# Kernel tuning notes

Measured on AMD Instinct MI355X. Metric: run time of the kernel, lower is better.

The kernel has to match this reference:

```python
import jax, jax.numpy as jnp
import numpy as np

B, N, P, D, K = 32, 512, 25, 128, 64
PROMPT_THRESHOLD = 0.5
T_MTI = 24  # last time patch is masked (module asserts t_mti == [24])


def setup_inputs() -> dict:
    key = jax.random.key(0)
    k1, k2, k3, k4, k5 = jax.random.split(key, 5)
    patches = jax.random.normal(k1, (B, N, P, D), dtype=jnp.float32)
    # kaiming-uniform-like init scale for the embedding tables
    scale = 1.0 / np.sqrt(D)
    u_prompt = jax.random.normal(k2, (K, D), dtype=jnp.float32) * scale
    m_prompt = jax.random.normal(k3, (K, D), dtype=jnp.float32) * scale
    s_mti = jnp.sort(jax.random.randint(k4, (256,), 0, N))
    s_uti = jnp.sort(jax.random.randint(k5, (256,), 0, N))
    return {"patches": patches, "u_prompt": u_prompt, "m_prompt": m_prompt,
            "s_mti": s_mti, "s_uti": s_uti}


def reference(patches, u_prompt, m_prompt, s_mti, s_uti):
    n, p = patches.shape[1], patches.shape[2]
    # multiplicative masks equivalent to score_map[:, s_mti] = 0 and score_map[:, :, 24] = 0
    n_mask = jnp.ones((n,), dtype=patches.dtype).at[s_mti].set(0.0)
    t_mask = jnp.ones((p,), dtype=patches.dtype).at[T_MTI].set(0.0)
    keep = (n_mask[:, None] * t_mask[None, :])[None, :, :, None]  # [1,N,P,1]

    # --- unmasked-prompt pass ---
    su = jax.nn.sigmoid(jnp.einsum('bnpd,kd->bnpk', patches, u_prompt))
    su = su * (su > PROMPT_THRESHOLD).astype(su.dtype) * keep
    out = patches + jnp.einsum('bnpk,kd->bnpd', su, u_prompt)

    # --- masked-prompt pass: score - score_with_keep == score * (1 - keep) ---
    sm = jax.nn.sigmoid(jnp.einsum('bnpd,kd->bnpk', patches, m_prompt))
    sm = sm * (sm > PROMPT_THRESHOLD).astype(sm.dtype) * (1.0 - keep)
    out = out + jnp.einsum('bnpk,kd->bnpd', sm, m_prompt)
    return out
```

## Files before the change

kernel.cpp:

```cpp
#include <hip/hip_runtime.h>


constexpr int NN = 512;
constexpr int PP = 25;
constexpr int DD = 128;
constexpr int KK = 64;
constexpr int THREADS = 512;
constexpr int ROWS = 32 * NN * PP;
constexpr int RPB = THREADS / 4;
constexpr int BLOCKS = ROWS / RPB;

__global__ __launch_bounds__(THREADS, 2)
void ape_kernel(const float* __restrict__ patches,
                const float* __restrict__ u_prompt,
                const float* __restrict__ m_prompt,
                const int* __restrict__ s_mti,
                float* __restrict__ out)
{
    __shared__ float S[2 * KK * DD];
    __shared__ unsigned nmask[NN / 32];

    const int tid = threadIdx.x;
    float4* S4 = reinterpret_cast<float4*>(S);

    if (tid < NN / 32) nmask[tid] = 0u;
    __syncthreads();
    if (tid < 256) {
        int idx = s_mti[tid];
        atomicOr(&nmask[idx >> 5], 1u << (idx & 31));
    }

    {
        const float4* u4 = reinterpret_cast<const float4*>(u_prompt);
        const float4* m4 = reinterpret_cast<const float4*>(m_prompt);
#pragma unroll
        for (int i = 0; i < 4; ++i) {
            int jj = i * THREADS + tid;
            int k = jj >> 5, j = jj & 31;
            int phys = (j & 24) | ((j ^ (j >> 3)) & 7);
            S4[k * 32 + phys]        = u4[jj];
            S4[2048 + k * 32 + phys] = m4[jj];
        }
    }
    __syncthreads();

    const int q = tid & 3;
    const int rl = tid >> 2;
    const int r = blockIdx.x * RPB + rl;
    const int rdp = r / PP;
    const int pp = r - rdp * PP;
    const int n = rdp & (NN - 1);
    const bool masked = (((nmask[n >> 5] >> (n & 31)) & 1u) != 0u) || (pp == 24);
    const int tb = masked ? 2048 : 0;

    int ecol[8];
#pragma unroll
    for (int t = 0; t < 8; ++t) ecol[t] = tb + q * 8 + ((t ^ q) & 7);

    const float4* pr = reinterpret_cast<const float4*>(patches) + (size_t)r * 32 + q * 8;
    float4 row[8], acc[8];
#pragma unroll
    for (int t = 0; t < 8; ++t) {
        row[t] = pr[t];
        acc[t] = row[t];
    }

#pragma unroll 1
    for (int k = 0; k < KK; ++k) {
        const int kb = k * 32;
        float4 e[8];
        float a0 = 0.f, a1 = 0.f, a2 = 0.f, a3 = 0.f;
#pragma unroll
        for (int t = 0; t < 8; ++t) {
            e[t] = S4[kb + ecol[t]];
            a0 = fmaf(row[t].x, e[t].x, a0);
            a1 = fmaf(row[t].y, e[t].y, a1);
            a2 = fmaf(row[t].z, e[t].z, a2);
            a3 = fmaf(row[t].w, e[t].w, a3);
        }
        float lg = (a0 + a1) + (a2 + a3);
        lg += __shfl_xor(lg, 1);
        lg += __shfl_xor(lg, 2);

        float g;
        if (__any(__builtin_fabsf(lg) < 1e-3f)) {
            double dd = 0.0;
#pragma unroll
            for (int t = 0; t < 8; ++t) {
                dd = fma((double)row[t].x, (double)e[t].x, dd);
                dd = fma((double)row[t].y, (double)e[t].y, dd);
                dd = fma((double)row[t].z, (double)e[t].z, dd);
                dd = fma((double)row[t].w, (double)e[t].w, dd);
            }
            dd += __shfl_xor(dd, 1);
            dd += __shfl_xor(dd, 2);
            if (fabs(dd) < 4e-5) {
                g = 0.25f;
            } else if (dd > 0.0) {
                g = __builtin_amdgcn_rcpf(1.0f + __expf(-lg));
            } else {
                g = 0.0f;
            }
        } else {
            g = (lg > 0.0f) ? __builtin_amdgcn_rcpf(1.0f + __expf(-lg)) : 0.0f;
        }

#pragma unroll
        for (int t = 0; t < 8; ++t) {
            acc[t].x = fmaf(g, e[t].x, acc[t].x);
            acc[t].y = fmaf(g, e[t].y, acc[t].y);
            acc[t].z = fmaf(g, e[t].z, acc[t].z);
            acc[t].w = fmaf(g, e[t].w, acc[t].w);
        }
    }

    __syncthreads();
    {
        const int r7 = rl & 7;
        const int wb = rl * 32 + q * 8;
#pragma unroll
        for (int t = 0; t < 8; ++t)
            S4[wb + ((t ^ q ^ r7) & 7)] = acc[t];
    }
    __syncthreads();
    {
        float4* out4 = reinterpret_cast<float4*>(out) + (size_t)blockIdx.x * (RPB * 32);
#pragma unroll
        for (int i = 0; i < 8; ++i) {
            int flat = i * THREADS + tid;
            int rr = flat >> 5, c = flat & 31;
            int qq = c >> 3, tt = c & 7;
            out4[flat] = S4[rr * 32 + qq * 8 + ((tt ^ qq ^ (rr & 7)) & 7)];
        }
    }
}

extern "C" void kernel_launch(void* const* d_in, const int* in_sizes, int n_in,
                              void* d_out, int out_size, void* d_ws, size_t ws_size,
                              hipStream_t stream) {
    const float* patches  = (const float*)d_in[0];
    const float* u_prompt = (const float*)d_in[1];
    const float* m_prompt = (const float*)d_in[2];
    const int*   s_mti    = (const int*)d_in[3];
    float* outp = (float*)d_out;

    ape_kernel<<<BLOCKS, THREADS, 0, stream>>>(patches, u_prompt, m_prompt, s_mti, outp);
}
```

Before: 659.7 us.

## Process two rows per thread sharing the same prompt table to reuse LDS loads

Each thread now handles a pair of rows that share the same mask state (patch j and j+12 of the same (b,n), or the p=24 patches of two adjacent groups). Each LDS prompt vector load is then reused for two dot products and two accumulations, halving LDS traffic per row and halving block count. The shared-memory staged coalesced output write is replaced by direct strided float4 stores from registers. Register pressure roughly doubles for row/acc arrays, which may reduce occupancy or cause spills under the 512-thread launch bound.

```diff
diff --git a/kernel.cpp b/kernel.cpp
--- a/kernel.cpp
+++ b/kernel.cpp
@@ -6,9 +6,10 @@
 constexpr int DD = 128;
 constexpr int KK = 64;
 constexpr int THREADS = 512;
-constexpr int ROWS = 32 * NN * PP;
-constexpr int RPB = THREADS / 4;
-constexpr int BLOCKS = ROWS / RPB;
+constexpr int PAIRS_A = 32 * NN * 12;
+constexpr int PAIRS_B = 32 * NN / 2;
+constexpr int PPB = THREADS / 4;
+constexpr int BLOCKS = (PAIRS_A + PAIRS_B) / PPB;
 
 __global__ __launch_bounds__(THREADS, 2)
 void ape_kernel(const float* __restrict__ patches,
@@ -45,24 +46,35 @@
     __syncthreads();
 
     const int q = tid & 3;
-    const int rl = tid >> 2;
-    const int r = blockIdx.x * RPB + rl;
-    const int rdp = r / PP;
-    const int pp = r - rdp * PP;
-    const int n = rdp & (NN - 1);
-    const bool masked = (((nmask[n >> 5] >> (n & 31)) & 1u) != 0u) || (pp == 24);
+    const int P = blockIdx.x * PPB + (tid >> 2);
+    int r0, r1;
+    bool masked;
+    if (P < PAIRS_A) {
+        int g = P / 12;
+        int j = P - 12 * g;
+        r0 = g * 25 + j;
+        r1 = r0 + 12;
+        int n = g & (NN - 1);
+        masked = (((nmask[n >> 5] >> (n & 31)) & 1u) != 0u);
+    } else {
+        int Qp = P - PAIRS_A;
+        r0 = (2 * Qp) * 25 + 24;
+        r1 = r0 + 25;
+        masked = true;
+    }
     const int tb = masked ? 2048 : 0;
 
     int ecol[8];
 #pragma unroll
     for (int t = 0; t < 8; ++t) ecol[t] = tb + q * 8 + ((t ^ q) & 7);
 
-    const float4* pr = reinterpret_cast<const float4*>(patches) + (size_t)r * 32 + q * 8;
-    float4 row[8], acc[8];
+    const float4* p0 = reinterpret_cast<const float4*>(patches) + (size_t)r0 * 32 + q * 8;
+    const float4* p1 = reinterpret_cast<const float4*>(patches) + (size_t)r1 * 32 + q * 8;
+    float4 row0[8], row1[8], acc0[8], acc1[8];
 #pragma unroll
     for (int t = 0; t < 8; ++t) {
-        row[t] = pr[t];
-        acc[t] = row[t];
+        row0[t] = p0[t]; acc0[t] = row0[t];
+        row1[t] = p1[t]; acc1[t] = row1[t];
     }
 
 #pragma unroll 1
@@ -70,68 +82,68 @@
         const int kb = k * 32;
         float4 e[8];
         float a0 = 0.f, a1 = 0.f, a2 = 0.f, a3 = 0.f;
+        float b0 = 0.f, b1 = 0.f, b2 = 0.f, b3 = 0.f;
 #pragma unroll
         for (int t = 0; t < 8; ++t) {
             e[t] = S4[kb + ecol[t]];
-            a0 = fmaf(row[t].x, e[t].x, a0);
-            a1 = fmaf(row[t].y, e[t].y, a1);
-            a2 = fmaf(row[t].z, e[t].z, a2);
-            a3 = fmaf(row[t].w, e[t].w, a3);
+            a0 = fmaf(row0[t].x, e[t].x, a0);
+            a1 = fmaf(row0[t].y, e[t].y, a1);
+            a2 = fmaf(row0[t].z, e[t].z, a2);
+            a3 = fmaf(row0[t].w, e[t].w, a3);
+            b0 = fmaf(row1[t].x, e[t].x, b0);
+            b1 = fmaf(row1[t].y, e[t].y, b1);
+            b2 = fmaf(row1[t].z, e[t].z, b2);
+            b3 = fmaf(row1[t].w, e[t].w, b3);
         }
-        float lg = (a0 + a1) + (a2 + a3);
-        lg += __shfl_xor(lg, 1);
-        lg += __shfl_xor(lg, 2);
+        float lg0 = (a0 + a1) + (a2 + a3);
+        float lg1 = (b0 + b1) + (b2 + b3);
+        lg0 += __shfl_xor(lg0, 1);  lg0 += __shfl_xor(lg0, 2);
+        lg1 += __shfl_xor(lg1, 1);  lg1 += __shfl_xor(lg1, 2);
 
-        float g;
-        if (__any(__builtin_fabsf(lg) < 1e-3f)) {
-            double dd = 0.0;
+        float g0, g1;
+        if (__any(fminf(__builtin_fabsf(lg0), __builtin_fabsf(lg1)) < 1e-3f)) {
+            double d0 = 0.0, d1 = 0.0;
 #pragma unroll
             for (int t = 0; t < 8; ++t) {
-                dd = fma((double)row[t].x, (double)e[t].x, dd);
-                dd = fma((double)row[t].y, (double)e[t].y, dd);
-                dd = fma((double)row[t].z, (double)e[t].z, dd);
-                dd = fma((double)row[t].w, (double)e[t].w, dd);
+                d0 = fma((double)row0[t].x, (double)e[t].x, d0);
+                d0 = fma((double)row0[t].y, (double)e[t].y, d0);
+                d0 = fma((double)row0[t].z, (double)e[t].z, d0);
+                d0 = fma((double)row0[t].w, (double)e[t].w, d0);
+                d1 = fma((double)row1[t].x, (double)e[t].x, d1);
+                d1 = fma((double)row1[t].y, (double)e[t].y, d1);
+                d1 = fma((double)row1[t].z, (double)e[t].z, d1);
+                d1 = fma((double)row1[t].w, (double)e[t].w, d1);
             }
-            dd += __shfl_xor(dd, 1);
-            dd += __shfl_xor(dd, 2);
-            if (fabs(dd) < 4e-5) {
-                g = 0.25f;
-            } else if (dd > 0.0) {
-                g = __builtin_amdgcn_rcpf(1.0f + __expf(-lg));
-            } else {
-                g = 0.0f;
-            }
+            d0 += __shfl_xor(d0, 1);  d0 += __shfl_xor(d0, 2);
+            d1 += __shfl_xor(d1, 1);  d1 += __shfl_xor(d1, 2);
+            g0 = (fabs(d0) < 4e-5) ? 0.25f
+               : (d0 > 0.0) ? __builtin_amdgcn_rcpf(1.0f + __expf(-lg0)) : 0.0f;
+            g1 = (fabs(d1) < 4e-5) ? 0.25f
+               : (d1 > 0.0) ? __builtin_amdgcn_rcpf(1.0f + __expf(-lg1)) : 0.0f;
         } else {
-            g = (lg > 0.0f) ? __builtin_amdgcn_rcpf(1.0f + __expf(-lg)) : 0.0f;
+            g0 = (lg0 > 0.0f) ? __builtin_amdgcn_rcpf(1.0f + __expf(-lg0)) : 0.0f;
+            g1 = (lg1 > 0.0f) ? __builtin_amdgcn_rcpf(1.0f + __expf(-lg1)) : 0.0f;
         }
 
 #pragma unroll
         for (int t = 0; t < 8; ++t) {
-            acc[t].x = fmaf(g, e[t].x, acc[t].x);
-            acc[t].y = fmaf(g, e[t].y, acc[t].y);
-            acc[t].z = fmaf(g, e[t].z, acc[t].z);
-            acc[t].w = fmaf(g, e[t].w, acc[t].w);
+            acc0[t].x = fmaf(g0, e[t].x, acc0[t].x);
+            acc0[t].y = fmaf(g0, e[t].y, acc0[t].y);
+            acc0[t].z = fmaf(g0, e[t].z, acc0[t].z);
+            acc0[t].w = fmaf(g0, e[t].w, acc0[t].w);
+            acc1[t].x = fmaf(g1, e[t].x, acc1[t].x);
+            acc1[t].y = fmaf(g1, e[t].y, acc1[t].y);
+            acc1[t].z = fmaf(g1, e[t].z, acc1[t].z);
+            acc1[t].w = fmaf(g1, e[t].w, acc1[t].w);
         }
     }
 
-    __syncthreads();
-    {
-        const int r7 = rl & 7;
-        const int wb = rl * 32 + q * 8;
+    float4* o0 = reinterpret_cast<float4*>(out) + (size_t)r0 * 32 + q * 8;
+    float4* o1 = reinterpret_cast<float4*>(out) + (size_t)r1 * 32 + q * 8;
 #pragma unroll
-        for (int t = 0; t < 8; ++t)
-            S4[wb + ((t ^ q ^ r7) & 7)] = acc[t];
-    }
-    __syncthreads();
-    {
-        float4* out4 = reinterpret_cast<float4*>(out) + (size_t)blockIdx.x * (RPB * 32);
-#pragma unroll
-        for (int i = 0; i < 8; ++i) {
-            int flat = i * THREADS + tid;
-            int rr = flat >> 5, c = flat & 31;
-            int qq = c >> 3, tt = c & 7;
-            out4[flat] = S4[rr * 32 + qq * 8 + ((tt ^ qq ^ (rr & 7)) & 7)];
-        }
+    for (int t = 0; t < 8; ++t) {
+        o0[t] = acc0[t];
+        o1[t] = acc1[t];
     }
 }
 
```

Result: faster. 637.8 us (-3.3%).
